# Optimization experiments

Measured on AMD Instinct MI355X. Metric: run time of the kernel, lower is better.

Reference implementation:

```python
import jax, jax.numpy as jnp
import numpy as np
from jax import lax

STRIDE = 6  # from init_kwargs


def setup_inputs() -> dict:
    key = jax.random.key(0)
    # spike-like activations in [0, 1); feature maps [F, H, W]
    s = jax.random.uniform(key, (128, 384, 384), dtype=jnp.float32)
    return {"s": s}


def reference(s):
    # Faithful to PoolingConnection.compute: for output (k, i, j) it takes
    #   max(s[k, i*stride : i*stride + h, j*stride : j*stride + w])
    # where h = H // stride, w = W // stride (NOT pooling_size -- that arg
    # is unused in the original code). Python slicing clips at the array
    # boundary, which equals right/bottom padding with -inf under a max.
    F, H, W = s.shape
    h, w = H // STRIDE, W // STRIDE
    pad_h = (h - 1) * STRIDE + h - H  # so that output height == h
    pad_w = (w - 1) * STRIDE + w - W
    out = lax.reduce_window(
        s,
        -jnp.inf,
        lax.max,
        window_dimensions=(1, h, w),
        window_strides=(1, STRIDE, STRIDE),
        padding=[(0, 0), (0, pad_h), (0, pad_w)],
    )  # [F, h, w]
    return out
```

## Files before the change

kernel.cpp:

```cpp
#include <hip/hip_runtime.h>
#include <math.h>


constexpr int F  = 128;
constexpr int H  = 384;
constexpr int W  = 384;
constexpr int ST = 6;
constexpr int OH = 64;
constexpr int OW = 64;

#define NINF (-__builtin_huge_valf())

__device__ __forceinline__ float sh_ninf(float v, int lane, int d) {
    float r = __shfl(v, lane + d, 64);
    return (lane + d > 63) ? NINF : r;
}

__global__ __launch_bounds__(1024) void pool_fused_kernel(const float* __restrict__ s,
                                                          float* __restrict__ out) {
    __shared__ float rowmax[250][64];
    __shared__ float segm[42][64];
    __shared__ float segp[42][64];

    const int k     = blockIdx.x >> 1;
    const int half  = blockIdx.x & 1;
    const int i0    = half * 32;
    const int rbeg  = i0 * ST;
    const int nrows = half ? (H - 192) : 250;

    const int tid  = threadIdx.x;
    const int wv   = tid >> 6;
    const int lane = tid & 63;

    const float* srow_base = s + ((size_t)k * H + rbeg) * W + lane * 6;
    for (int rl = wv; rl < nrows; rl += 16) {
        const float* row = srow_base + (size_t)rl * W;
        const float2 e0 = *reinterpret_cast<const float2*>(row);
        const float2 e1 = *reinterpret_cast<const float2*>(row + 2);
        const float2 e2 = *reinterpret_cast<const float2*>(row + 4);

        const float p3 = fmaxf(fmaxf(e0.x, e0.y), fmaxf(e1.x, e1.y));
        const float m  = fmaxf(p3, fmaxf(e2.x, e2.y));

        const float a1 = fmaxf(m,  sh_ninf(m,  lane, 1));
        const float a2 = fmaxf(a1, sh_ninf(a1, lane, 2));
        const float a3 = fmaxf(a2, sh_ninf(a2, lane, 4));
        const float a4 = fmaxf(a3, sh_ninf(a1, lane, 8));
        const float r  = fmaxf(a4, sh_ninf(p3, lane, 10));

        rowmax[rl][lane] = r;
    }
    __syncthreads();

    for (int job = tid; job < 42 * 64; job += 1024) {
        const int gl = job >> 6;
        const int j  = job & 63;
        const int r0 = gl * 6;
        float m6 = NINF, m4 = NINF;
        #pragma unroll
        for (int t = 0; t < 6; ++t) {
            const float v = (r0 + t < nrows) ? rowmax[r0 + t][j] : NINF;
            m6 = fmaxf(m6, v);
            if (t < 4) m4 = fmaxf(m4, v);
        }
        segm[gl][j] = m6;
        segp[gl][j] = m4;
    }
    __syncthreads();

    for (int job = tid; job < 32 * 64; job += 1024) {
        const int li = job >> 6;
        const int j  = job & 63;
        float acc = segp[li + 10][j];
        #pragma unroll
        for (int t = 0; t < 10; ++t) acc = fmaxf(acc, segm[li + t][j]);
        out[((size_t)k * OH + i0 + li) * OW + j] = acc;
    }
}

extern "C" void kernel_launch(void* const* d_in, const int* in_sizes, int n_in,
                              void* d_out, int out_size, void* d_ws, size_t ws_size,
                              hipStream_t stream) {
    const float* s = (const float*)d_in[0];
    float* out     = (float*)d_out;
    pool_fused_kernel<<<F * 2, 1024, 0, stream>>>(s, out);
}
```

Baseline: 19.77 us.

## Reduce rows vertically per segment before the horizontal sliding max

Each warp now loads the six rows of a stride segment and reduces them in registers. It applies the shuffle-based horizontal sliding-window max once per segment, for the 6-row and 4-row partials, instead of once per input row. This removes the per-row rowmax shared buffer, one reduction pass and one barrier, and cuts shuffle work. The two blocks per feature map are also rebalanced so each reads 37 segments, at the cost of padding the segment buffers with -inf tail rows.

Result: faster. 18.54 us (-6.2%).

```diff
diff --git a/kernel.cpp b/kernel.cpp
--- a/kernel.cpp
+++ b/kernel.cpp
@@ -9,6 +9,9 @@
 constexpr int OH = 64;
 constexpr int OW = 64;
 
+constexpr int NSEG   = 37;
+constexpr int SEGPAD = NSEG + 10;
+
 #define NINF (-__builtin_huge_valf())
 
 __device__ __forceinline__ float sh_ninf(float v, int lane, int d) {
@@ -16,65 +19,66 @@
     return (lane + d > 63) ? NINF : r;
 }
 
+__device__ __forceinline__ float slide_window(float m, float p3, int lane) {
+    const float a1 = fmaxf(m,  sh_ninf(m,  lane, 1));
+    const float a2 = fmaxf(a1, sh_ninf(a1, lane, 2));
+    const float a3 = fmaxf(a2, sh_ninf(a2, lane, 4));
+    const float a4 = fmaxf(a3, sh_ninf(a1, lane, 8));
+    return fmaxf(a4, sh_ninf(p3, lane, 10));
+}
+
 __global__ __launch_bounds__(1024) void pool_fused_kernel(const float* __restrict__ s,
                                                           float* __restrict__ out) {
-    __shared__ float rowmax[250][64];
-    __shared__ float segm[42][64];
-    __shared__ float segp[42][64];
+    __shared__ float segm[SEGPAD][64];
+    __shared__ float segp[SEGPAD][64];
 
-    const int k     = blockIdx.x >> 1;
-    const int half  = blockIdx.x & 1;
-    const int i0    = half * 32;
-    const int rbeg  = i0 * ST;
-    const int nrows = half ? (H - 192) : 250;
+    const int k    = blockIdx.x >> 1;
+    const int half = blockIdx.x & 1;
+
+    const int sbeg = half ? 27 : 0;
+    const int obeg = half ? 27 : 0;
+    const int ni   = half ? 37 : 27;
 
     const int tid  = threadIdx.x;
     const int wv   = tid >> 6;
     const int lane = tid & 63;
 
-    const float* srow_base = s + ((size_t)k * H + rbeg) * W + lane * 6;
-    for (int rl = wv; rl < nrows; rl += 16) {
-        const float* row = srow_base + (size_t)rl * W;
-        const float2 e0 = *reinterpret_cast<const float2*>(row);
-        const float2 e1 = *reinterpret_cast<const float2*>(row + 2);
-        const float2 e2 = *reinterpret_cast<const float2*>(row + 4);
+    for (int job = tid; job < 10 * 64; job += 1024) {
+        const int g = NSEG + (job >> 6);
+        const int j = job & 63;
+        segm[g][j] = NINF;
+        segp[g][j] = NINF;
+    }
 
-        const float p3 = fmaxf(fmaxf(e0.x, e0.y), fmaxf(e1.x, e1.y));
-        const float m  = fmaxf(p3, fmaxf(e2.x, e2.y));
-
-        const float a1 = fmaxf(m,  sh_ninf(m,  lane, 1));
-        const float a2 = fmaxf(a1, sh_ninf(a1, lane, 2));
-        const float a3 = fmaxf(a2, sh_ninf(a2, lane, 4));
-        const float a4 = fmaxf(a3, sh_ninf(a1, lane, 8));
-        const float r  = fmaxf(a4, sh_ninf(p3, lane, 10));
-
-        rowmax[rl][lane] = r;
+    const float* base = s + ((size_t)k * H + sbeg * ST) * W + lane * 6;
+    for (int gl = wv; gl < NSEG; gl += 16) {
+        const float* seg = base + (size_t)gl * ST * W;
+        float vm6 = NINF, vp6 = NINF;
+        float vm4 = NINF, vp4 = NINF;
+        #pragma unroll
+        for (int t = 0; t < 6; ++t) {
+            const float* row = seg + (size_t)t * W;
+            const float2 e0 = *reinterpret_cast<const float2*>(row);
+            const float2 e1 = *reinterpret_cast<const float2*>(row + 2);
+            const float2 e2 = *reinterpret_cast<const float2*>(row + 4);
+            const float p3 = fmaxf(fmaxf(e0.x, e0.y), fmaxf(e1.x, e1.y));
+            const float m  = fmaxf(p3, fmaxf(e2.x, e2.y));
+            vm6 = fmaxf(vm6, m);
+            vp6 = fmaxf(vp6, p3);
+            if (t < 4) { vm4 = fmaxf(vm4, m); vp4 = fmaxf(vp4, p3); }
+        }
+        segm[gl][lane] = slide_window(vm6, vp6, lane);
+        segp[gl][lane] = slide_window(vm4, vp4, lane);
     }
     __syncthreads();
 
-    for (int job = tid; job < 42 * 64; job += 1024) {
-        const int gl = job >> 6;
-        const int j  = job & 63;
-        const int r0 = gl * 6;
-        float m6 = NINF, m4 = NINF;
-        #pragma unroll
-        for (int t = 0; t < 6; ++t) {
-            const float v = (r0 + t < nrows) ? rowmax[r0 + t][j] : NINF;
-            m6 = fmaxf(m6, v);
-            if (t < 4) m4 = fmaxf(m4, v);
-        }
-        segm[gl][j] = m6;
-        segp[gl][j] = m4;
-    }
-    __syncthreads();
-
-    for (int job = tid; job < 32 * 64; job += 1024) {
+    for (int job = tid; job < ni * 64; job += 1024) {
         const int li = job >> 6;
         const int j  = job & 63;
         float acc = segp[li + 10][j];
         #pragma unroll
         for (int t = 0; t < 10; ++t) acc = fmaxf(acc, segm[li + t][j]);
-        out[((size_t)k * OH + i0 + li) * OW + j] = acc;
+        out[((size_t)k * OH + obeg + li) * OW + j] = acc;
     }
 }
 
```
